# Kernel tuning notes

Measured on AMD Instinct MI355X. Metric: run time of the kernel, lower is better.

The kernel has to match this reference:

```python
import jax, jax.numpy as jnp
import numpy as np

EMBED_DIM = 256
NUM_EMBED = 1024
COMMIT_COST = 0.25


def setup_inputs() -> dict:
    key = jax.random.key(0)
    kx, kc = jax.random.split(key)
    x = jax.random.normal(kx, (64, 32, 32, EMBED_DIM), dtype=jnp.float32)
    codebook = jax.random.normal(kc, (NUM_EMBED, EMBED_DIM), dtype=jnp.float32)
    return {"x": x, "codebook": codebook}


def reference(x, codebook):
    # flatten to [N, D]
    flat_x = x.reshape(-1, EMBED_DIM)
    distances = (
        jnp.sum(flat_x ** 2, axis=1, keepdims=True)
        + jnp.sum(codebook ** 2, axis=1)
        - 2.0 * jnp.matmul(flat_x, codebook.T)
    )
    encoding_indices = jnp.argmin(distances, axis=1)  # [N]
    quantized = codebook[encoding_indices].reshape(x.shape)
    # losses (detach semantics via stop_gradient)
    q_latent_loss = jnp.mean((quantized - jax.lax.stop_gradient(x)) ** 2)
    e_latent_loss = jnp.mean((x - jax.lax.stop_gradient(quantized)) ** 2)
    loss = q_latent_loss + COMMIT_COST * e_latent_loss
    # straight-through estimator
    quantized = x + jax.lax.stop_gradient(quantized - x)
    return (quantized, loss)
```

## Files before the change

### kernel.cpp

```cpp
#include <hip/hip_runtime.h>

#define D 256
#define K 1024
#define NVEC 65536
#define ROWS 32
#define GROUPC 256
#define NG (K / GROUPC)
#define NKB (D / 32)
#define MARGIN 0.5f
#define MAXC 12
#define MAXP (ROWS * MAXC)

typedef __attribute__((ext_vector_type(8))) __bf16 bf16x8;
typedef __attribute__((ext_vector_type(4))) float floatx4;

__device__ inline unsigned short f2bf(float f) {
    unsigned int u = __float_as_uint(f);
    unsigned int r = u + 0x7fffu + ((u >> 16) & 1u);
    return (unsigned short)(r >> 16);
}
__device__ inline unsigned int fkey(float f) {
    unsigned int b = __float_as_uint(f);
    return (b & 0x80000000u) ? ~b : (b | 0x80000000u);
}
__device__ inline float unfkey(unsigned int k) {
    unsigned int b = (k & 0x80000000u) ? (k & 0x7fffffffu) : ~k;
    return __uint_as_float(b);
}


__global__ void vq_prep(const float* __restrict__ cb, float* __restrict__ cnorm,
                        unsigned short* __restrict__ cbf, float* __restrict__ lossAcc) {
    const int c = blockIdx.x;
    const int l = threadIdx.x;
    float4 v = *(const float4*)&cb[c * D + l * 4];
    float s = v.x * v.x + v.y * v.y + v.z * v.z + v.w * v.w;
#pragma unroll
    for (int off = 32; off > 0; off >>= 1) s += __shfl_down(s, off, 64);
    if (l == 0) cnorm[c] = s;
    const int g = c >> 8, w = (c >> 6) & 3, j = (c >> 4) & 3, col = c & 15;
    const int kb = l >> 3, quad = (l >> 1) & 3, h = (l & 1) * 4;
    const int S = ((g * 8 + kb) * 4 + w) * 4 + j;
    *(ushort4*)(cbf + (size_t)S * 512 + (quad * 16 + col) * 8 + h) =
        make_ushort4(f2bf(v.x), f2bf(v.y), f2bf(v.z), f2bf(v.w));
    if (c == 0 && l == 0) *lossAcc = 0.f;
}

__global__ __launch_bounds__(256, 5) void vq_fused(
        const float* __restrict__ x, const float* __restrict__ cb,
        const unsigned short* __restrict__ cbf, const float* __restrict__ cnorm,
        float* __restrict__ lossAcc, float* __restrict__ out)
{
    __shared__ __align__(16) unsigned short xs[ROWS * D];
    __shared__ unsigned int rowMinU[ROWS];
    __shared__ unsigned long long rowBest[ROWS];
    __shared__ int ccnt[ROWS];
    __shared__ int cand[ROWS][MAXC];
    __shared__ int pairs[MAXP];
    __shared__ int pcnt;
    __shared__ int widx[ROWS];
    __shared__ float wsum[4];

    const int tid = threadIdx.x;
    const int wave = tid >> 6;
    const int lane = tid & 63;
    const int quad = lane >> 4;
    const int col  = lane & 15;
    const int rowBase = blockIdx.x * ROWS;
    const float* xblk = x + (size_t)rowBase * D;

    if (tid < ROWS) { rowMinU[tid] = 0xFFFFFFFFu; rowBest[tid] = ~0ull; ccnt[tid] = 0; }
    if (tid == 0) pcnt = 0;

#pragma unroll
    for (int it = 0; it < ROWS * D / 4 / 256; ++it) {
        int e = tid + it * 256;
        int r = e >> 6;
        int d4 = (e & 63) << 2;
        float4 v = *(const float4*)&xblk[r * D + d4];
        int slot = (d4 >> 3) ^ (r & 31);
        *(ushort4*)&xs[r * D + slot * 8 + (d4 & 4)] =
            make_ushort4(f2bf(v.x), f2bf(v.y), f2bf(v.z), f2bf(v.w));
    }
    __syncthreads();

    for (int g = 0; g < NG; ++g) {
        floatx4 acc[2][4];
#pragma unroll
        for (int i = 0; i < 2; ++i)
#pragma unroll
            for (int j = 0; j < 4; ++j) acc[i][j] = (floatx4){0.f, 0.f, 0.f, 0.f};

#pragma unroll
        for (int kb = 0; kb < NKB; ++kb) {
            bf16x8 af[2], bfr[4];
#pragma unroll
            for (int i = 0; i < 2; ++i) {
                int r = i * 16 + col;
                int slot = (kb * 4 + quad) ^ (r & 31);
                af[i] = *(const bf16x8*)&xs[r * D + slot * 8];
            }
#pragma unroll
            for (int j = 0; j < 4; ++j) {
                int S = ((g * 8 + kb) * 4 + wave) * 4 + j;
                bfr[j] = *(const bf16x8*)(cbf + (size_t)S * 512 + lane * 8);
            }
#pragma unroll
            for (int j = 0; j < 4; ++j)
#pragma unroll
                for (int i = 0; i < 2; ++i)
                    acc[i][j] = __builtin_amdgcn_mfma_f32_16x16x32_bf16(af[i], bfr[j], acc[i][j], 0, 0, 0);
        }

        const int cbase = g * GROUPC + wave * 64;
        float cn[4];
#pragma unroll
        for (int j = 0; j < 4; ++j) cn[j] = cnorm[cbase + j * 16 + col];

#pragma unroll
        for (int i = 0; i < 2; ++i)
#pragma unroll
            for (int reg = 0; reg < 4; ++reg) {
                float v = cn[0] - 2.f * acc[i][0][reg];
#pragma unroll
                for (int j = 1; j < 4; ++j)
                    v = fminf(v, cn[j] - 2.f * acc[i][j][reg]);
#pragma unroll
                for (int off = 1; off < 16; off <<= 1)
                    v = fminf(v, __shfl_xor(v, off, 64));
                if (col == 0)
                    atomicMin(&rowMinU[i * 16 + quad * 4 + reg], fkey(v));
            }
        __syncthreads();
#pragma unroll
        for (int i = 0; i < 2; ++i)
#pragma unroll
            for (int reg = 0; reg < 4; ++reg) {
                int row = i * 16 + quad * 4 + reg;
                float lim = unfkey(rowMinU[row]) + MARGIN;
#pragma unroll
                for (int j = 0; j < 4; ++j) {
                    float d2 = cn[j] - 2.f * acc[i][j][reg];
                    if (d2 < lim) {
                        int slot = atomicAdd(&ccnt[row], 1);
                        if (slot < MAXC) cand[row][slot] = cbase + j * 16 + col;
                    }
                }
            }
    }
    __syncthreads();

    if (tid < ROWS) {
        int m = ccnt[tid]; if (m > MAXC) m = MAXC;
        for (int c = 0; c < m; ++c) {
            int p = atomicAdd(&pcnt, 1);
            pairs[p] = (tid << 10) | cand[tid][c];
        }
    }
    __syncthreads();
    const int np = pcnt;

    const int team = wave * 4 + quad;
    for (int p = team; p < np; p += 16) {
        int pr = pairs[p];
        int row = pr >> 10, code = pr & 1023;
        const float* xr = xblk + row * D + col * 16;
        const float* er = cb + (size_t)code * D + col * 16;
        float s = 0.f;
#pragma unroll
        for (int q = 0; q < 4; ++q) {
            float4 a = *(const float4*)(xr + q * 4);
            float4 b = *(const float4*)(er + q * 4);
            s += a.x * b.x + a.y * b.y + a.z * b.z + a.w * b.w;
        }
#pragma unroll
        for (int off = 1; off < 16; off <<= 1) s += __shfl_xor(s, off, 64);
        if (col == 0) {
            float dist = cnorm[code] - 2.f * s;
            unsigned long long pack = ((unsigned long long)fkey(dist) << 32) | (unsigned int)code;
            atomicMin(&rowBest[row], pack);
        }
    }

    for (int rr = 0; rr < ROWS / 4; ++rr) {
        const int rl = wave * (ROWS / 4) + rr;
        if (ccnt[rl] > MAXC) {
            float best = 3.4e38f;
            int bi = 0x7fffffff;
            for (int c = lane; c < K; c += 64) {
                float p = 0.f;
                for (int k = 0; k < D; ++k) p += xblk[rl * D + k] * cb[(size_t)c * D + k];
                float dist = cnorm[c] - 2.f * p;
                if (dist < best || (dist == best && c < bi)) { best = dist; bi = c; }
            }
#pragma unroll
            for (int off = 1; off < 64; off <<= 1) {
                float ob = __shfl_xor(best, off, 64);
                int oi = __shfl_xor(bi, off, 64);
                if (ob < best || (ob == best && oi < bi)) { best = ob; bi = oi; }
            }
            if (lane == 0)
                atomicMin(&rowBest[rl], ((unsigned long long)fkey(best) << 32) | (unsigned int)bi);
        }
    }
    __syncthreads();
    if (tid < ROWS) widx[tid] = (int)(rowBest[tid] & 0xffffffffu);
    __syncthreads();

    float part = 0.f;
#pragma unroll
    for (int it = 0; it < ROWS * D / 4 / 256; ++it) {
        int e4 = tid + it * 256;
        int r = e4 >> 6, d4 = (e4 & 63) * 4;
        float4 q = *(const float4*)&cb[(size_t)widx[r] * D + d4];
        float4 xv = *(const float4*)&xblk[r * D + d4];
        *(float4*)&out[(size_t)rowBase * D + r * D + d4] = q;
        float a = q.x - xv.x, b = q.y - xv.y, c2 = q.z - xv.z, d2 = q.w - xv.w;
        part += a * a + b * b + c2 * c2 + d2 * d2;
    }
#pragma unroll
    for (int off = 32; off > 0; off >>= 1) part += __shfl_down(part, off, 64);
    if (lane == 0) wsum[wave] = part;
    __syncthreads();
    if (tid == 0) atomicAdd(lossAcc, wsum[0] + wsum[1] + wsum[2] + wsum[3]);
}

__global__ void vq_final_kernel(const float* __restrict__ lossAcc, float* __restrict__ outLoss) {
    *outLoss = 1.25f * (*lossAcc) / 16777216.f;
}

extern "C" void kernel_launch(void* const* d_in, const int* in_sizes, int n_in,
                              void* d_out, int out_size, void* d_ws, size_t ws_size,
                              hipStream_t stream) {
    const float* x  = (const float*)d_in[0];
    const float* cb = (const float*)d_in[1];
    float* out = (float*)d_out;

    float* cnorm = (float*)d_ws;
    float* lossAcc = cnorm + K;
    unsigned short* cbf = (unsigned short*)((char*)d_ws + 8192);

    vq_prep<<<K, 64, 0, stream>>>(cb, cnorm, cbf, lossAcc);
    vq_fused<<<NVEC / ROWS, 256, 0, stream>>>(x, cb, cbf, cnorm, lossAcc, out);
    vq_final_kernel<<<1, 1, 0, stream>>>(lossAcc, out + (size_t)NVEC * D);
}
```

Before: 231.4 us.

## Keep x tile in LDS as fp32 and reuse it for rescoring and loss

The x tile is now staged in shared memory as fp32 instead of bf16, with a swizzled float4 layout, and converted to bf16 on the fly when MFMA fragments are loaded. The candidate rescoring, the full-scan fallback and the loss/output pass read x from LDS instead of re-reading global memory. This doubles the LDS footprint to 32KB per block, so the launch bound drops from 5 to 4 blocks, and it adds conversion work inside the MFMA inner loop.

Result: faster. 211.7 us (-8.5%).

```diff
diff --git a/kernel.cpp b/kernel.cpp
--- a/kernel.cpp
+++ b/kernel.cpp
@@ -27,6 +27,14 @@
     unsigned int b = (k & 0x80000000u) ? (k & 0x7fffffffu) : ~k;
     return __uint_as_float(b);
 }
+__device__ inline bf16x8 pack8(float4 a, float4 b) {
+    union { bf16x8 v; unsigned short u[8]; } t;
+    t.u[0] = f2bf(a.x); t.u[1] = f2bf(a.y); t.u[2] = f2bf(a.z); t.u[3] = f2bf(a.w);
+    t.u[4] = f2bf(b.x); t.u[5] = f2bf(b.y); t.u[6] = f2bf(b.z); t.u[7] = f2bf(b.w);
+    return t.v;
+}
+
+#define XSLOT(r, s) (((s) & 32) | (((s) & 31) ^ ((r) & 31)))
 
 
 __global__ void vq_prep(const float* __restrict__ cb, float* __restrict__ cnorm,
@@ -46,12 +54,12 @@
     if (c == 0 && l == 0) *lossAcc = 0.f;
 }
 
-__global__ __launch_bounds__(256, 5) void vq_fused(
+__global__ __launch_bounds__(256, 4) void vq_fused(
         const float* __restrict__ x, const float* __restrict__ cb,
         const unsigned short* __restrict__ cbf, const float* __restrict__ cnorm,
         float* __restrict__ lossAcc, float* __restrict__ out)
 {
-    __shared__ __align__(16) unsigned short xs[ROWS * D];
+    __shared__ __align__(16) float xs[ROWS * D];
     __shared__ unsigned int rowMinU[ROWS];
     __shared__ unsigned long long rowBest[ROWS];
     __shared__ int ccnt[ROWS];
@@ -76,11 +84,9 @@
     for (int it = 0; it < ROWS * D / 4 / 256; ++it) {
         int e = tid + it * 256;
         int r = e >> 6;
-        int d4 = (e & 63) << 2;
-        float4 v = *(const float4*)&xblk[r * D + d4];
-        int slot = (d4 >> 3) ^ (r & 31);
-        *(ushort4*)&xs[r * D + slot * 8 + (d4 & 4)] =
-            make_ushort4(f2bf(v.x), f2bf(v.y), f2bf(v.z), f2bf(v.w));
+        int s = e & 63;
+        float4 v = *(const float4*)&xblk[r * D + s * 4];
+        *(float4*)&xs[r * D + XSLOT(r, s) * 4] = v;
     }
     __syncthreads();
 
@@ -97,8 +103,11 @@
 #pragma unroll
             for (int i = 0; i < 2; ++i) {
                 int r = i * 16 + col;
-                int slot = (kb * 4 + quad) ^ (r & 31);
-                af[i] = *(const bf16x8*)&xs[r * D + slot * 8];
+                int s0 = kb * 8 + quad * 2;
+                int slot0 = XSLOT(r, s0);
+                float4 a = *(const float4*)&xs[r * D + slot0 * 4];
+                float4 b = *(const float4*)&xs[r * D + (slot0 ^ 1) * 4];
+                af[i] = pack8(a, b);
             }
 #pragma unroll
             for (int j = 0; j < 4; ++j) {
@@ -164,12 +173,12 @@
     for (int p = team; p < np; p += 16) {
         int pr = pairs[p];
         int row = pr >> 10, code = pr & 1023;
-        const float* xr = xblk + row * D + col * 16;
         const float* er = cb + (size_t)code * D + col * 16;
         float s = 0.f;
 #pragma unroll
         for (int q = 0; q < 4; ++q) {
-            float4 a = *(const float4*)(xr + q * 4);
+            int sg = col * 4 + q;
+            float4 a = *(const float4*)&xs[row * D + XSLOT(row, sg) * 4];
             float4 b = *(const float4*)(er + q * 4);
             s += a.x * b.x + a.y * b.y + a.z * b.z + a.w * b.w;
         }
@@ -189,7 +198,10 @@
             int bi = 0x7fffffff;
             for (int c = lane; c < K; c += 64) {
                 float p = 0.f;
-                for (int k = 0; k < D; ++k) p += xblk[rl * D + k] * cb[(size_t)c * D + k];
+                for (int k = 0; k < D; ++k) {
+                    int sg = k >> 2;
+                    p += xs[rl * D + XSLOT(rl, sg) * 4 + (k & 3)] * cb[(size_t)c * D + k];
+                }
                 float dist = cnorm[c] - 2.f * p;
                 if (dist < best || (dist == best && c < bi)) { best = dist; bi = c; }
             }
@@ -211,10 +223,10 @@
 #pragma unroll
     for (int it = 0; it < ROWS * D / 4 / 256; ++it) {
         int e4 = tid + it * 256;
-        int r = e4 >> 6, d4 = (e4 & 63) * 4;
-        float4 q = *(const float4*)&cb[(size_t)widx[r] * D + d4];
-        float4 xv = *(const float4*)&xblk[r * D + d4];
-        *(float4*)&out[(size_t)rowBase * D + r * D + d4] = q;
+        int r = e4 >> 6, s = e4 & 63;
+        float4 q = *(const float4*)&cb[(size_t)widx[r] * D + s * 4];
+        float4 xv = *(const float4*)&xs[r * D + XSLOT(r, s) * 4];
+        *(float4*)&out[(size_t)rowBase * D + r * D + s * 4] = q;
         float a = q.x - xv.x, b = q.y - xv.y, c2 = q.z - xv.z, d2 = q.w - xv.w;
         part += a * a + b * b + c2 * c2 + d2 * d2;
     }
```
